# Kernel tuning notes

Measured on AMD Instinct MI355X. Metric: run time of the kernel, lower is better.

Reference implementation:

```python
import jax, jax.numpy as jnp
import numpy as np

EPS = 1e-5

def layer_norm(x, w, b):
    mu = x.mean(-1, keepdims=True)
    var = x.var(-1, keepdims=True)
    return (x - mu) / jnp.sqrt(var + EPS) * w + b

def moe_ffn(y, gW, W1, b1, W2, b2, topk):
    # y: [B,N,d]; W1: [E,d,f]; W2: [E,f,d].  Dense-equivalent of the
    # torch gather/compute/scatter-add dispatch: every expert runs on every
    # token, combined with top-k gate weights (zero for unselected experts).
    gate = jax.nn.softmax(y @ gW, axis=-1)                       # [B,N,E]
    w, sel = jax.lax.top_k(gate, topk)                           # [B,N,k]
    onehot = jax.nn.one_hot(sel, gW.shape[-1], dtype=y.dtype)    # [B,N,k,E]
    comb = jnp.einsum('bnk,bnke->bne', w, onehot)                # combine weights
    hmid = jax.nn.gelu(jnp.einsum('bnd,edf->bnef', y, W1) + b1, approximate=False)
    eo = jnp.einsum('bnef,efd->bned', hmid, W2) + b2             # [B,N,E,d]
    out = jnp.einsum('bne,bned->bnd', comb, eo)
    mask = onehot.sum(2)                                         # [B,N,E] 0/1
    cnt = mask.sum((0, 1))                                       # tokens per expert
    emb = jnp.einsum('bne,bnd->ed', mask, y) / jnp.maximum(cnt, 1.0)[:, None]
    return out, gate, emb

def setup_inputs():
    B, S, N = 8, 512, 1024
    d, H, E, f, L, topk = 512, 8, 8, 8, 2, 2   # d_ff == n_heads (repo quirk)
    key = jax.random.key(0)
    ks = iter(jax.random.split(key, 40))
    g = lambda shape, s=0.02: jax.random.normal(next(ks), shape, jnp.float32) * s
    return dict(
        x=jax.random.normal(next(ks), (B, S, N), jnp.float32),
        revin_w=jnp.ones((N,), jnp.float32) + g((N,), 0.01),
        revin_b=g((N,), 0.01),
        emb_W=g((S, d)), emb_b=g((d,)),
        Wq=g((L, d, d)), bq=g((L, d)),
        Wk=g((L, d, d)), bk=g((L, d)),
        Wv=g((L, d, d)), bv=g((L, d)),
        Wo=g((L, d, d)), bo=g((L, d)),
        ln1_w=jnp.ones((L, d), jnp.float32), ln1_b=jnp.zeros((L, d), jnp.float32),
        ln2_w=jnp.ones((L, d), jnp.float32), ln2_b=jnp.zeros((L, d), jnp.float32),
        gate_W=g((L, d, E)),
        eW1=g((L, E, d, f)), eb1=g((L, E, f)),
        eW2=g((L, E, f, d)), eb2=g((L, E, d)),
        enc_norm_w=jnp.ones((d,), jnp.float32), enc_norm_b=jnp.zeros((d,), jnp.float32),
        head_gate_W=g((d, E)),
        head_W=g((E, d, d)), head_b=g((E, d)),
        topk=topk, n_heads=H,
    )

def reference(x, revin_w, revin_b, emb_W, emb_b, Wq, bq, Wk, bk, Wv, bv, Wo, bo,
              ln1_w, ln1_b, ln2_w, ln2_b, gate_W, eW1, eb1, eW2, eb2,
              enc_norm_w, enc_norm_b, head_gate_W, head_W, head_b, topk, n_heads):
    B, S, N = x.shape
    d = emb_W.shape[1]
    H = n_heads
    dh = d // H
    L = Wq.shape[0]
    # RevIN normalize over time per variable (dropout layers are eval/identity)
    xv = jnp.swapaxes(x, 1, 2)                                   # [B,N,S]
    mean = xv.mean(-1, keepdims=True)
    std = jnp.sqrt(xv.var(-1, keepdims=True) + EPS)
    xn = (xv - mean) / std * revin_w[None, :, None] + revin_b[None, :, None]
    # DataEmbedding_inverted: Linear over the time axis -> variable tokens
    h = xn @ emb_W + emb_b                                       # [B,N,d]
    for l in range(L):
        q = (h @ Wq[l] + bq[l]).reshape(B, N, H, dh)
        k = (h @ Wk[l] + bk[l]).reshape(B, N, H, dh)
        v = (h @ Wv[l] + bv[l]).reshape(B, N, H, dh)
        attn = jax.nn.softmax(jnp.einsum('bnhe,bmhe->bhnm', q, k) / jnp.sqrt(jnp.float32(dh)), axis=-1)
        o = jnp.einsum('bhnm,bmhe->bnhe', attn, v).reshape(B, N, d) @ Wo[l] + bo[l]
        h = layer_norm(h + o, ln1_w[l], ln1_b[l])
        ffn, _gate, _emb = moe_ffn(h, gate_W[l], eW1[l], eb1[l], eW2[l], eb2[l], topk)
        h = layer_norm(h + ffn, ln2_w[l], ln2_b[l])
    h = layer_norm(h, enc_norm_w, enc_norm_b)
    # MoE projection head: experts are Linear(d, d)
    gate = jax.nn.softmax(h @ head_gate_W, axis=-1)
    w, sel = jax.lax.top_k(gate, topk)
    onehot = jax.nn.one_hot(sel, head_gate_W.shape[-1], dtype=h.dtype)
    comb = jnp.einsum('bnk,bnke->bne', w, onehot)
    eo = jnp.einsum('bnd,edf->bnef', h, head_W) + head_b         # [B,N,E,d]
    out = jnp.einsum('bne,bned->bnd', comb, eo)                  # [B,N,d]
    # RevIN denorm applied on [B, d_model, N]
    o2 = jnp.swapaxes(out, 1, 2)
    o2 = (o2 - revin_b[None, None, :]) / (revin_w[None, None, :] + 1e-10)
    o2 = o2 * jnp.swapaxes(std, 1, 2) + jnp.swapaxes(mean, 1, 2)
    return jnp.swapaxes(o2, 1, 2)                                # [B, n_vars, d_model]
```

## Files before the change

kernel.cpp:

```cpp
#include <hip/hip_runtime.h>
#include <math.h>

#define BATCH 8
#define SEQ 512
#define NVAR 1024
#define DM 512
#define NH 8
#define DH 64
#define NE 8
#define NF 8
#define NL 2
#define NTOK (BATCH*NVAR)
#define LN_EPS 1e-5f
#define LSC 2048.0f
#define ILSC (1.0f/2048.0f)

typedef __attribute__((ext_vector_type(8))) _Float16 f16x8;
typedef __attribute__((ext_vector_type(4))) float f32x4;
#define MFMA16 __builtin_amdgcn_mfma_f32_16x16x32_f16

__device__ __forceinline__ void fsplit(float v, _Float16& hi, _Float16& lo) {
    hi = (_Float16)v;
    lo = (_Float16)((v - (float)hi) * LSC);
}
__device__ __forceinline__ float frec(_Float16 hi, _Float16 lo) {
    return (float)hi + (float)lo * ILSC;
}

__device__ __forceinline__ void gload_lds16(const _Float16* g, _Float16* l) {
    __builtin_amdgcn_global_load_lds(
        (const __attribute__((address_space(1))) void*)g,
        (__attribute__((address_space(3))) void*)l, 16, 0, 0);
}

#define DPPROR(v, C) __int_as_float(__builtin_amdgcn_update_dpp(0, __float_as_int(v), (C), 0xF, 0xF, true))
__device__ __forceinline__ float rowmax16(float v) {
    v = fmaxf(v, DPPROR(v, 0x121));
    v = fmaxf(v, DPPROR(v, 0x122));
    v = fmaxf(v, DPPROR(v, 0x124));
    v = fmaxf(v, DPPROR(v, 0x128));
    return v;
}
__device__ __forceinline__ float rowsum16(float v) {
    v += DPPROR(v, 0x121);
    v += DPPROR(v, 0x122);
    v += DPPROR(v, 0x124);
    v += DPPROR(v, 0x128);
    return v;
}
// ... 123 lines not shown
            }
        }
    }
    #undef G_STAGE
#pragma unroll
    for (int h2 = 0; h2 < 2; ++h2)
#pragma unroll
        for (int nt = 0; nt < 4; ++nt) {
            int col = bn + nt*16 + m16;
            float bv = bias[col];
#pragma unroll
            for (int r = 0; r < 4; ++r) {
                size_t row = bm + w*32 + h2*16 + quad*4 + r;
                float v = a1[h2][nt][r] + a2[h2][nt][r]*ILSC + bv;
                if (C) C[row*N + col] = v;
                if (Chi) {
                    _Float16 h_, l_; fsplit(v, h_, l_);
                    Chi[row*N + col] = h_; Clo[row*N + col] = l_;
                }
            }
        }
}

__global__ __launch_bounds__(256) void gemm_qk_kernel(
        const _Float16* __restrict__ Ahg, const _Float16* __restrict__ Alg,
        const _Float16* __restrict__ Whg, const _Float16* __restrict__ Wlg,
        const float* __restrict__ biasQ, const float* __restrict__ biasK,
        _Float16* __restrict__ Qhi, _Float16* __restrict__ Qlo,
        _Float16* __restrict__ KKhi, _Float16* __restrict__ KKlo) {
    __shared__ _Float16 smem[24576];
    int id = blockIdx.x;
    int rm = ((id & 7) << 7) | (id >> 3);
    int bm = (rm >> 4) << 7, bn = (rm & 15) << 6;
    int t = threadIdx.x;
    int w = t >> 6, lane = t & 63, m16 = lane & 15, quad = lane >> 4;
    int wv = __builtin_amdgcn_readfirstlane(w);
    int lrow = lane >> 2, lcol = (lane & 3) << 3;
    f32x4 a1[2][4] = {}, a2[2][4] = {};

    #define G_STAGE(c, kk) do {                                              \
        _Pragma("unroll")                                                    \
        for (int ch = 0; ch < 2; ++ch) {                                     \
            size_t ga = (size_t)(bm + wv*32 + ch*16 + lrow)*DM + (kk) + lcol;\
            gload_lds16(&Ahg[ga], &smem[(c)*4096 + (wv*32 + ch*16)*32]);     \
            gload_lds16(&Alg[ga], &smem[8192 + (c)*4096 + (wv*32 + ch*16)*32]); \
        }                                                                    \
        size_t gb = (size_t)(bn + wv*16 + lrow)*DM + (kk) + lcol;            \
        gload_lds16(&Whg[gb], &smem[16384 + (c)*2048 + (wv*16)*32]);         \
        gload_lds16(&Wlg[gb], &smem[20480 + (c)*2048 + (wv*16)*32]);         \
    } while (0)

    G_STAGE(0, 0);
    int cur = 0;
    for (int k0 = 0; k0 < DM; k0 += 32, cur ^= 1) {
        __syncthreads();
        if (k0 + 32 < DM) G_STAGE(cur ^ 1, k0 + 32);
        const _Float16* AH = &smem[cur*4096];
        const _Float16* AL = &smem[8192 + cur*4096];
        const _Float16* BH = &smem[16384 + cur*2048];
        const _Float16* BL = &smem[20480 + cur*2048];
        f16x8 bh_[4], bl_[4];
#pragma unroll
        for (int nt = 0; nt < 4; ++nt) {
            bh_[nt] = *(const f16x8*)&BH[(nt*16 + m16)*32 + quad*8];
            bl_[nt] = *(const f16x8*)&BL[(nt*16 + m16)*32 + quad*8];
        }
#pragma unroll
        for (int h2 = 0; h2 < 2; ++h2) {
            f16x8 ah = *(const f16x8*)&AH[(w*32 + h2*16 + m16)*32 + quad*8];
            f16x8 al = *(const f16x8*)&AL[(w*32 + h2*16 + m16)*32 + quad*8];
#pragma unroll
            for (int nt = 0; nt < 4; ++nt) {
                a1[h2][nt] = MFMA16(ah, bh_[nt], a1[h2][nt], 0, 0, 0);
                a2[h2][nt] = MFMA16(ah, bl_[nt], a2[h2][nt], 0, 0, 0);
                a2[h2][nt] = MFMA16(al, bh_[nt], a2[h2][nt], 0, 0, 0);
            }
        }
    }
    #undef G_STAGE
    const float* bias = (bn < 512) ? biasQ : biasK;
    _Float16* Ohi = (bn < 512) ? Qhi : KKhi;
    _Float16* Olo = (bn < 512) ? Qlo : KKlo;
    int cb = (bn < 512) ? bn : bn - 512;
#pragma unroll
    for (int h2 = 0; h2 < 2; ++h2)
#pragma unroll
        for (int nt = 0; nt < 4; ++nt) {
            int col = cb + nt*16 + m16;
            float bv = bias[col];
#pragma unroll
            for (int r = 0; r < 4; ++r) {
                size_t row = bm + w*32 + h2*16 + quad*4 + r;
                float v = a1[h2][nt][r] + a2[h2][nt][r]*ILSC + bv;
                _Float16 h_, l_; fsplit(v, h_, l_);
                Ohi[row*DM + col] = h_; Olo[row*DM + col] = l_;
            }
        }
}

__global__ __launch_bounds__(256) void gemm_f16x2_vt_kernel(
        const _Float16* __restrict__ Ahg, const _Float16* __restrict__ Alg,
        const _Float16* __restrict__ Whg, const _Float16* __restrict__ Wlg,
        const float* __restrict__ bias,
        _Float16* __restrict__ vthi, _Float16* __restrict__ vtlo) {
    __shared__ _Float16 smem[24576];
    int id = blockIdx.x + (blockIdx.y << 3);
    int rm = ((id & 7) << 6) | (id >> 3);
    int bm = (rm >> 3) << 7, bn = (rm & 7) << 6;
    int t = threadIdx.x;
    int w = t >> 6, lane = t & 63, m16 = lane & 15, quad = lane >> 4;
    int wv = __builtin_amdgcn_readfirstlane(w);
    int lrow = lane >> 2, lcol = (lane & 3) << 3;
    f32x4 a1[2][4] = {}, a2[2][4] = {};

    #define G_STAGE(c, kk) do {                                              \
        _Pragma("unroll")                                                    \
        for (int ch = 0; ch < 2; ++ch) {                                     \
            size_t ga = (size_t)(bm + wv*32 + ch*16 + lrow)*DM + (kk) + lcol;\
            gload_lds16(&Ahg[ga], &smem[(c)*4096 + (wv*32 + ch*16)*32]);     \
            gload_lds16(&Alg[ga], &smem[8192 + (c)*4096 + (wv*32 + ch*16)*32]); \
        }                                                                    \
        size_t gb = (size_t)(bn + wv*16 + lrow)*DM + (kk) + lcol;            \
        gload_lds16(&Whg[gb], &smem[16384 + (c)*2048 + (wv*16)*32]);         \
        gload_lds16(&Wlg[gb], &smem[20480 + (c)*2048 + (wv*16)*32]);         \
    } while (0)

    G_STAGE(0, 0);
    int cur = 0;
    for (int k0 = 0; k0 < DM; k0 += 32, cur ^= 1) {
        __syncthreads();
        if (k0 + 32 < DM) G_STAGE(cur ^ 1, k0 + 32);
        const _Float16* AH = &smem[cur*4096];
        const _Float16* AL = &smem[8192 + cur*4096];
        const _Float16* BH = &smem[16384 + cur*2048];
        const _Float16* BL = &smem[20480 + cur*2048];
        f16x8 bh_[4], bl_[4];
#pragma unroll
        for (int nt = 0; nt < 4; ++nt) {
            bh_[nt] = *(const f16x8*)&BH[(nt*16 + m16)*32 + quad*8];
            bl_[nt] = *(const f16x8*)&BL[(nt*16 + m16)*32 + quad*8];
        }
#pragma unroll
        for (int h2 = 0; h2 < 2; ++h2) {
            f16x8 ah = *(const f16x8*)&AH[(w*32 + h2*16 + m16)*32 + quad*8];
            f16x8 al = *(const f16x8*)&AL[(w*32 + h2*16 + m16)*32 + quad*8];
#pragma unroll
            for (int nt = 0; nt < 4; ++nt) {
                a1[h2][nt] = MFMA16(ah, bh_[nt], a1[h2][nt], 0, 0, 0);
                a2[h2][nt] = MFMA16(ah, bl_[nt], a2[h2][nt], 0, 0, 0);
                a2[h2][nt] = MFMA16(al, bh_[nt], a2[h2][nt], 0, 0, 0);
            }
        }
    }
    #undef G_STAGE
    __syncthreads();
    float (*Ct)[65] = (float (*)[65])smem;
#pragma unroll
    for (int h2 = 0; h2 < 2; ++h2)
#pragma unroll
        for (int nt = 0; nt < 4; ++nt) {
            float bv = bias[bn + nt*16 + m16];
#pragma unroll
            for (int r = 0; r < 4; ++r)
                Ct[w*32 + h2*16 + quad*4 + r][nt*16 + m16] = a1[h2][nt][r] + a2[h2][nt][r]*ILSC + bv;
        }
    __syncthreads();
    int b = bm >> 10, tokn0 = bm & 1023, hh = bn >> 6;
    int dh = t >> 2, tg = (t & 3) << 4;
    size_t rowb = ((size_t)(b*8 + hh)*64 + dh)*NVAR + tokn0;
    for (int hb = 0; hb < 2; ++hb) {
        int tl0 = hb*64 + tg;
        unsigned short hbuf[16], lbuf[16];
#pragma unroll
        for (int i = 0; i < 16; ++i) {
            _Float16 h_, l_; fsplit(Ct[tl0 + i][dh], h_, l_);
            hbuf[i] = __builtin_bit_cast(unsigned short, h_);
            lbuf[i] = __builtin_bit_cast(unsigned short, l_);
        }
        uint4 uh0, uh1, ul0, ul1;
        uh0.x = hbuf[0]|(hbuf[1]<<16);  uh0.y = hbuf[2]|(hbuf[3]<<16);
        uh0.z = hbuf[4]|(hbuf[5]<<16);  uh0.w = hbuf[6]|(hbuf[7]<<16);
        uh1.x = hbuf[8]|(hbuf[9]<<16);  uh1.y = hbuf[10]|(hbuf[11]<<16);
        uh1.z = hbuf[12]|(hbuf[13]<<16);uh1.w = hbuf[14]|(hbuf[15]<<16);
        ul0.x = lbuf[0]|(lbuf[1]<<16);  ul0.y = lbuf[2]|(lbuf[3]<<16);
        ul0.z = lbuf[4]|(lbuf[5]<<16);  ul0.w = lbuf[6]|(lbuf[7]<<16);
        ul1.x = lbuf[8]|(lbuf[9]<<16);  ul1.y = lbuf[10]|(lbuf[11]<<16);
        ul1.z = lbuf[12]|(lbuf[13]<<16);ul1.w = lbuf[14]|(lbuf[15]<<16);
        *(uint4*)&vthi[rowb + tl0]     = uh0;
        *(uint4*)&vthi[rowb + tl0 + 8] = uh1;
        *(uint4*)&vtlo[rowb + tl0]     = ul0;
        *(uint4*)&vtlo[rowb + tl0 + 8] = ul1;
    }
}

__global__ __launch_bounds__(256, 4) void attn_f16x2_kernel(
        const _Float16* __restrict__ qh, const _Float16* __restrict__ ql,
        const _Float16* __restrict__ kh, const _Float16* __restrict__ kl,
        const _Float16* __restrict__ vth, const _Float16* __restrict__ vtl,
        _Float16* __restrict__ oh, _Float16* __restrict__ ol) {
    __shared__ _Float16 Kh[64][72], Kl[64][72];
    __shared__ _Float16 Vh[64][72], Vl[64][72];
    int blk = blockIdx.x;
    blk = ((blk & 7) << 7) | (blk >> 3);
    int qt = blk & 15, bh = blk >> 4;
    int b = bh >> 3, hh = bh & 7;
    int q0 = qt << 6;
    int t = threadIdx.x;
    int w = t >> 6, lane = t & 63;
    int m16 = lane & 15, quad = lane >> 4;
    size_t bbase = (size_t)b * NVAR;
    size_t vbase = (size_t)bh * DH * NVAR;

    f16x8 qfh[2], qfl[2];
#pragma unroll
// ... 49 lines not shown
        if (__any(grow)) {
#pragma unroll
            for (int r = 0; r < 4; ++r) {
                float mnew = fmaxf(mrow[r], mx[r]);
                float alpha = __expf(mrow[r] - mnew);
                mrow[r] = mnew;
                lrow[r] *= alpha;
#pragma unroll
                for (int nt = 0; nt < 4; ++nt) { o1[nt][r] *= alpha; o2[nt][r] *= alpha; }
            }
        }
#pragma unroll
        for (int r = 0; r < 4; ++r) {
            float p0 = __expf(pbuf[0][r] - mrow[r]);
            float p1 = __expf(pbuf[1][r] - mrow[r]);
            float p2 = __expf(pbuf[2][r] - mrow[r]);
            float p3 = __expf(pbuf[3][r] - mrow[r]);
            lrow[r] += rowsum16(p0 + p1 + p2 + p3);
            pbuf[0][r] = p0; pbuf[1][r] = p1; pbuf[2][r] = p2; pbuf[3][r] = p3;
        }
#pragma unroll
        for (int nt = 0; nt < 4; ++nt)
#pragma unroll
            for (int r = 0; r < 4; ++r) {
                _Float16 h_, l_; fsplit(pbuf[nt][r], h_, l_);
                Kh[w*16 + quad*4 + r][nt*16 + m16] = h_;
                Kl[w*16 + quad*4 + r][nt*16 + m16] = l_;
            }

#pragma unroll
        for (int ks = 0; ks < 2; ++ks) {
            f16x8 ph = *(const f16x8*)&Kh[w*16 + m16][ks*32 + quad*8];
            f16x8 pl = *(const f16x8*)&Kl[w*16 + m16][ks*32 + quad*8];
#pragma unroll
            for (int nt = 0; nt < 4; ++nt) {
                f16x8 vh_ = *(const f16x8*)&Vh[nt*16 + m16][ks*32 + quad*8];
                f16x8 vl_ = *(const f16x8*)&Vl[nt*16 + m16][ks*32 + quad*8];
                o1[nt] = MFMA16(ph, vh_, o1[nt], 0, 0, 0);
                o2[nt] = MFMA16(ph, vl_, o2[nt], 0, 0, 0);
                o2[nt] = MFMA16(pl, vh_, o2[nt], 0, 0, 0);
            }
        }
        __syncthreads();
    }
#pragma unroll
    for (int r = 0; r < 4; ++r) {
        float inv = 1.0f / lrow[r];
        size_t rowp = (bbase + q0 + w*16 + quad*4 + r)*DM + hh*DH;
#pragma unroll
        for (int nt = 0; nt < 4; ++nt) {
            float ov = fmaf(o2[nt][r], ILSC, o1[nt][r]) * inv;
            _Float16 h_, l_; fsplit(ov, h_, l_);
            oh[rowp + nt*16 + m16] = h_;
            ol[rowp + nt*16 + m16] = l_;
        }
    }
}

__global__ __launch_bounds__(256) void ln_kernel(
        _Float16* __restrict__ hhi, _Float16* __restrict__ hlo,
        const float* __restrict__ res,
        const float* __restrict__ w, const float* __restrict__ b) {
    int rowi = blockIdx.x, t = threadIdx.x;
    size_t base = (size_t)rowi * DM;
    int c = t << 1;
    unsigned int uh = *(const unsigned int*)&hhi[base + c];
    unsigned int ul = *(const unsigned int*)&hlo[base + c];
    _Float16 h0 = __builtin_bit_cast(_Float16, (unsigned short)(uh & 0xFFFF));
    _Float16 h1 = __builtin_bit_cast(_Float16, (unsigned short)(uh >> 16));
    _Float16 l0 = __builtin_bit_cast(_Float16, (unsigned short)(ul & 0xFFFF));
    _Float16 l1 = __builtin_bit_cast(_Float16, (unsigned short)(ul >> 16));
    float v0 = frec(h0, l0);
    float v1 = frec(h1, l1);
    if (res) { float2 rv = *(const float2*)&res[base + c]; v0 += rv.x; v1 += rv.y; }
    float s = v0 + v1, q = v0*v0 + v1*v1;
#pragma unroll
    for (int off = 1; off < 64; off <<= 1) {
        s += __shfl_xor(s, off);
        q += __shfl_xor(q, off);
    }
    __shared__ float sred[4], qred[4];
    int wid = t >> 6, lane = t & 63;
    if (lane == 0) { sred[wid] = s; qred[wid] = q; }
    __syncthreads();
    s = sred[0] + sred[1] + sred[2] + sred[3];
    q = qred[0] + qred[1] + qred[2] + qred[3];
    float m = s / (float)DM;
    float var = q / (float)DM - m*m;
    float inv = 1.0f / sqrtf(var + LN_EPS);
    float2 wv = *(const float2*)&w[c];
    float2 bv = *(const float2*)&b[c];
    float y0 = (v0 - m)*inv * wv.x + bv.x;
    float y1 = (v1 - m)*inv * wv.y + bv.y;
    _Float16 h0o, l0o, h1o, l1o;
    fsplit(y0, h0o, l0o); fsplit(y1, h1o, l1o);
    *(unsigned int*)&hhi[base + c] =
        (unsigned int)__builtin_bit_cast(unsigned short, h0o) |
        ((unsigned int)__builtin_bit_cast(unsigned short, h1o) << 16);
    *(unsigned int*)&hlo[base + c] =
        (unsigned int)__builtin_bit_cast(unsigned short, l0o) |
        ((unsigned int)__builtin_bit_cast(unsigned short, l1o) << 16);
}

__device__ __forceinline__ float gelu_exact(float xv) {
    return 0.5f * xv * (1.0f + erff(xv * 0.70710678118654752f));
}

__global__ __launch_bounds__(256) void moe_ln_kernel(
        _Float16* __restrict__ hhi, _Float16* __restrict__ hlo,
        const float* __restrict__ gW, const float* __restrict__ W1, const float* __restrict__ b1,
        const float* __restrict__ W2, const float* __restrict__ b2,
        const float* __restrict__ lw, const float* __restrict__ lb) {
    int tok = blockIdx.x, t = threadIdx.x;
    __shared__ float hs[DM];
    __shared__ float red[32][8];
    __shared__ float glog[8];
    __shared__ float hmid[8];
    __shared__ float wsel[2];
    __shared__ int   esel[2];
    __shared__ float sred[4], qred[4];
    size_t base = (size_t)tok * DM;
    int c = t << 1;
    unsigned int uh = *(const unsigned int*)&hhi[base + c];
    unsigned int ul = *(const unsigned int*)&hlo[base + c];
    float hv0 = frec(__builtin_bit_cast(_Float16, (unsigned short)(uh & 0xFFFF)),
                     __builtin_bit_cast(_Float16, (unsigned short)(ul & 0xFFFF)));
    float hv1 = frec(__builtin_bit_cast(_Float16, (unsigned short)(uh >> 16)),
                     __builtin_bit_cast(_Float16, (unsigned short)(ul >> 16)));
    hs[c] = hv0; hs[c + 1] = hv1;
    __syncthreads();
    int e = t & 7, i0 = t >> 3;
    {
        float a = 0.f;
        for (int i = i0; i < DM; i += 32) a += hs[i] * gW[i*NE + e];
        red[i0][e] = a;
    }
    __syncthreads();
    if (t < 8) { float sv = 0.f; for (int i = 0; i < 32; ++i) sv += red[i][t]; glog[t] = sv; }
    __syncthreads();
    if (t == 0) {
        float m0 = -1e30f, m1 = -1e30f; int s0i = 0, s1i = 0;
        for (int ei = 0; ei < 8; ++ei) {
            float vv = glog[ei];
            if (vv > m0) { m1 = m0; s1i = s0i; m0 = vv; s0i = ei; }
            else if (vv > m1) { m1 = vv; s1i = ei; }
        }
        float Z = 0.f;
        for (int ei = 0; ei < 8; ++ei) Z += expf(glog[ei] - m0);
        wsel[0] = 1.0f / Z;
        wsel[1] = expf(m1 - m0) / Z;
        esel[0] = s0i; esel[1] = s1i;
// ... 23 lines not shown
        }
        o0 += wk * s0v; o1 += wk * s1v;
        __syncthreads();
    }
    float v0 = hv0 + o0, v1 = hv1 + o1;
    float s = v0 + v1, q = v0*v0 + v1*v1;
#pragma unroll
    for (int off = 1; off < 64; off <<= 1) {
        s += __shfl_xor(s, off);
        q += __shfl_xor(q, off);
    }
    int wid = t >> 6, lane = t & 63;
    if (lane == 0) { sred[wid] = s; qred[wid] = q; }
    __syncthreads();
    s = sred[0] + sred[1] + sred[2] + sred[3];
    q = qred[0] + qred[1] + qred[2] + qred[3];
    float m = s / (float)DM;
    float var = q / (float)DM - m*m;
    float inv = 1.0f / sqrtf(var + LN_EPS);
    float2 wv = *(const float2*)&lw[c];
    float2 bv = *(const float2*)&lb[c];
    float y0 = (v0 - m)*inv * wv.x + bv.x;
    float y1 = (v1 - m)*inv * wv.y + bv.y;
    _Float16 h0o, l0o, h1o, l1o;
    fsplit(y0, h0o, l0o); fsplit(y1, h1o, l1o);
    *(unsigned int*)&hhi[base + c] =
        (unsigned int)__builtin_bit_cast(unsigned short, h0o) |
        ((unsigned int)__builtin_bit_cast(unsigned short, h1o) << 16);
    *(unsigned int*)&hlo[base + c] =
        (unsigned int)__builtin_bit_cast(unsigned short, l0o) |
        ((unsigned int)__builtin_bit_cast(unsigned short, l1o) << 16);
}

__global__ __launch_bounds__(256) void encln_gate_kernel(
        _Float16* __restrict__ hhi, _Float16* __restrict__ hlo,
        const float* __restrict__ lw, const float* __restrict__ lb,
        const float* __restrict__ gW,
        int* __restrict__ sel, float2* __restrict__ wpair) {
    int tok = blockIdx.x, t = threadIdx.x;
    __shared__ float hs[DM];
    __shared__ float red[32][8];
    __shared__ float glog[8];
    __shared__ float sred[4], qred[4];
    size_t base = (size_t)tok * DM;
    int c = t << 1;
    unsigned int uh = *(const unsigned int*)&hhi[base + c];
    unsigned int ul = *(const unsigned int*)&hlo[base + c];
    float v0 = frec(__builtin_bit_cast(_Float16, (unsigned short)(uh & 0xFFFF)),
                    __builtin_bit_cast(_Float16, (unsigned short)(ul & 0xFFFF)));
    float v1 = frec(__builtin_bit_cast(_Float16, (unsigned short)(uh >> 16)),
                    __builtin_bit_cast(_Float16, (unsigned short)(ul >> 16)));
    float s = v0 + v1, q = v0*v0 + v1*v1;
#pragma unroll
    for (int off = 1; off < 64; off <<= 1) {
        s += __shfl_xor(s, off);
        q += __shfl_xor(q, off);
    }
    int wid = t >> 6, lane = t & 63;
    if (lane == 0) { sred[wid] = s; qred[wid] = q; }
    __syncthreads();
    s = sred[0] + sred[1] + sred[2] + sred[3];
    q = qred[0] + qred[1] + qred[2] + qred[3];
    float m = s / (float)DM;
    float var = q / (float)DM - m*m;
    float inv = 1.0f / sqrtf(var + LN_EPS);
    float2 wv = *(const float2*)&lw[c];
    float2 bv = *(const float2*)&lb[c];
    float y0 = (v0 - m)*inv * wv.x + bv.x;
    float y1 = (v1 - m)*inv * wv.y + bv.y;
    _Float16 h0o, l0o, h1o, l1o;
    fsplit(y0, h0o, l0o); fsplit(y1, h1o, l1o);
    *(unsigned int*)&hhi[base + c] =
        (unsigned int)__builtin_bit_cast(unsigned short, h0o) |
        ((unsigned int)__builtin_bit_cast(unsigned short, h1o) << 16);
    *(unsigned int*)&hlo[base + c] =
        (unsigned int)__builtin_bit_cast(unsigned short, l0o) |
        ((unsigned int)__builtin_bit_cast(unsigned short, l1o) << 16);
    hs[c] = y0; hs[c + 1] = y1;
    __syncthreads();
    int e = t & 7, i0 = t >> 3;
    float a = 0.f;
    for (int i = i0; i < DM; i += 32) a += hs[i] * gW[i*NE + e];
    red[i0][e] = a;
    __syncthreads();
    if (t < 8) { float sv = 0.f; for (int i = 0; i < 32; ++i) sv += red[i][t]; glog[t] = sv; }
    __syncthreads();
    if (t == 0) {
        float m0 = -1e30f, m1 = -1e30f; int s0i = 0, s1i = 0;
        for (int ei = 0; ei < 8; ++ei) {
            float vv = glog[ei];
            if (vv > m0) { m1 = m0; s1i = s0i; m0 = vv; s0i = ei; }
            else if (vv > m1) { m1 = vv; s1i = ei; }
        }
        float Z = 0.f;
        for (int ei = 0; ei < 8; ++ei) Z += __expf(glog[ei] - m0);
        float2 wvv;
        wvv.x = 1.0f / Z;
        wvv.y = __expf(m1 - m0) / Z;
        sel[tok] = s0i | (s1i << 3);
        wpair[tok] = wvv;
    }
}

__global__ __launch_bounds__(64) void head_init_kernel(int* __restrict__ cnt) {
    if (threadIdx.x < NE) cnt[threadIdx.x] = 0;
}

__global__ __launch_bounds__(64) void head_bucket_kernel(
        const int* __restrict__ sel, const float2* __restrict__ wpair,
        int* __restrict__ cnt, int* __restrict__ idxlist, float* __restrict__ wlist,
        int* __restrict__ pos0, int* __restrict__ pos1) {
    int lane = threadIdx.x;
    int tok = blockIdx.x*64 + lane;
    int s = sel[tok];
    int s0 = s & 7, s1 = (s >> 3) & 7;
    float2 wv = wpair[tok];
    unsigned long long lmask = (lane == 63) ? 0x7FFFFFFFFFFFFFFFull
                                            : ((1ull << lane) - 1ull);
#pragma unroll
    for (int e = 0; e < NE; ++e) {
        unsigned long long m0 = __ballot(s0 == e);
        unsigned long long m1 = __ballot(s1 == e);
        int tot = __popcll(m0) + __popcll(m1);
        int basep = 0;
        if (lane == 0 && tot > 0) basep = atomicAdd(&cnt[e], tot);
        basep = __shfl(basep, 0);
        if (s0 == e) {
            int p = basep + __popcll(m0 & lmask);
// ... 184 lines not shown
    dim3 ggemm(DM/64, NTOK/128);

    revin_stats_kernel<<<dim3(BATCH*16), blk, 0, stream>>>(x, mean, stdd);
    revin_norm_kernel<<<dim3(NVAR/32, SEQ/32, BATCH), blk, 0, stream>>>(
        x, mean, stdd, revin_w, revin_b, qhi, qlo);

    WSrcs srcs;
    srcs.p[0] = emb_W;
    for (int l = 0; l < NL; ++l) {
        srcs.p[1 + l*4 + 0] = Wq + (size_t)l*DM*DM;
        srcs.p[1 + l*4 + 1] = Wk + (size_t)l*DM*DM;
        srcs.p[1 + l*4 + 2] = Wv + (size_t)l*DM*DM;
        srcs.p[1 + l*4 + 3] = Wo + (size_t)l*DM*DM;
    }
    transpose_w_kernel<<<dim3(8, 8, 9), blk, 0, stream>>>(srcs, whi, wlo);

    gemm_f16x2_kernel<<<ggemm, blk, 0, stream>>>(
        qhi, qlo, whi, wlo, emb_b, nullptr, hhi, hlo, NTOK, SEQ, DM);

    for (int l = 0; l < NL; ++l) {
        size_t oq = (size_t)(1 + l*4 + 0)*DM*DM;
        size_t ov = (size_t)(1 + l*4 + 2)*DM*DM;
        size_t oo = (size_t)(1 + l*4 + 3)*DM*DM;
        gemm_qk_kernel<<<dim3(1024), blk, 0, stream>>>(
            hhi, hlo, whi + oq, wlo + oq, bq + l*DM, bk + l*DM,
            qhi, qlo, khi, klo);
        gemm_f16x2_vt_kernel<<<ggemm, blk, 0, stream>>>(
            hhi, hlo, whi + ov, wlo + ov, bv + l*DM, vthi, vtlo);
        attn_f16x2_kernel<<<dim3(64*16), blk, 0, stream>>>(
            qhi, qlo, khi, klo, vthi, vtlo, qhi, qlo);
        gemm_f16x2_kernel<<<ggemm, blk, 0, stream>>>(
            qhi, qlo, whi + oo, wlo + oo, bo + l*DM, proj, nullptr, nullptr, NTOK, DM, DM);
        ln_kernel<<<dim3(NTOK), blk, 0, stream>>>(hhi, hlo, proj, ln1_w + l*DM, ln1_b + l*DM);
        moe_ln_kernel<<<dim3(NTOK), blk, 0, stream>>>(
            hhi, hlo, gate_W + (size_t)l*DM*NE,
            eW1 + (size_t)l*NE*DM*NF, eb1 + (size_t)l*NE*NF,
            eW2 + (size_t)l*NE*NF*DM, eb2 + (size_t)l*NE*DM,
            ln2_w + l*DM, ln2_b + l*DM);
    }

    WSrcs hsrcs;
    for (int e = 0; e < NE; ++e) hsrcs.p[e] = hW + (size_t)e*DM*DM;
    hsrcs.p[8] = hW;
    transpose_w_kernel<<<dim3(8, 8, 8), blk, 0, stream>>>(hsrcs, vthi, vtlo);

    head_init_kernel<<<dim3(1), dim3(64), 0, stream>>>(cnt);
    encln_gate_kernel<<<dim3(NTOK), blk, 0, stream>>>(
        hhi, hlo, enc_w, enc_b, hgW, sel, wpair);
    head_bucket_kernel<<<dim3(NTOK/64), dim3(64), 0, stream>>>(
        sel, wpair, cnt, idxlist, wlist, pos0, pos1);
    head_prefix_kernel<<<dim3(1), dim3(64), 0, stream>>>(cnt);
    head_gemm_f16x2_kernel<<<dim3(576), blk, 0, stream>>>(
        hhi, hlo, vthi, vtlo, hb, cnt, idxlist, wlist, slotf);
    head_combine_kernel<<<dim3(NTOK), blk, 0, stream>>>(
        slotf, pos0, pos1, cnt, revin_w, revin_b, mean, stdd, out);
}
```

Before: 812.3 us.

## Fuse QK and V projection GEMMs into one launch, pack f16 splits

Merges the Q/K GEMM and the transposed-V GEMM into a single kernel that chooses its path by block index, removing one launch per layer and improving tail occupancy. Replaces scalar hi/lo f16 splitting with packed cvt_pkrtz conversions in the attention, layernorm and gate kernels. Folds the expert-counter zeroing into the encoder-norm gate kernel, dropping a tiny launch. The packed conversion rounds toward zero, which slightly changes the hi/lo split.

```diff
diff --git a/kernel.cpp b/kernel.cpp
--- a/kernel.cpp
+++ b/kernel.cpp
@@ -16,6 +16,7 @@
 #define ILSC (1.0f/2048.0f)
 
 typedef __attribute__((ext_vector_type(8))) _Float16 f16x8;
+typedef __attribute__((ext_vector_type(2))) _Float16 f16x2;
 typedef __attribute__((ext_vector_type(4))) float f32x4;
 #define MFMA16 __builtin_amdgcn_mfma_f32_16x16x32_f16
 
@@ -25,6 +26,11 @@
 }
 __device__ __forceinline__ float frec(_Float16 hi, _Float16 lo) {
     return (float)hi + (float)lo * ILSC;
+}
+__device__ __forceinline__ void fsplit2(float a, float b, f16x2& h2, f16x2& l2) {
+    h2 = __builtin_bit_cast(f16x2, __builtin_amdgcn_cvt_pkrtz(a, b));
+    l2 = __builtin_bit_cast(f16x2, __builtin_amdgcn_cvt_pkrtz(
+             (a - (float)h2.x)*LSC, (b - (float)h2.y)*LSC));
 }
 
 __device__ __forceinline__ void gload_lds16(const _Float16* g, _Float16* l) {
@@ -194,174 +200,167 @@
         }
 }
 
-__global__ __launch_bounds__(256) void gemm_qk_kernel(
+__global__ __launch_bounds__(256) void gemm_qkvt_kernel(
         const _Float16* __restrict__ Ahg, const _Float16* __restrict__ Alg,
-        const _Float16* __restrict__ Whg, const _Float16* __restrict__ Wlg,
+        const _Float16* __restrict__ Wqkh, const _Float16* __restrict__ Wqkl,
+        const _Float16* __restrict__ Wvh,  const _Float16* __restrict__ Wvl,
         const float* __restrict__ biasQ, const float* __restrict__ biasK,
+        const float* __restrict__ biasV,
         _Float16* __restrict__ Qhi, _Float16* __restrict__ Qlo,
-        _Float16* __restrict__ KKhi, _Float16* __restrict__ KKlo) {
+        _Float16* __restrict__ KKhi, _Float16* __restrict__ KKlo,
+        _Float16* __restrict__ vthi, _Float16* __restrict__ vtlo) {
     __shared__ _Float16 smem[24576];
-    int id = blockIdx.x;
-    int rm = ((id & 7) << 7) | (id >> 3);
-    int bm = (rm >> 4) << 7, bn = (rm & 15) << 6;
     int t = threadIdx.x;
     int w = t >> 6, lane = t & 63, m16 = lane & 15, quad = lane >> 4;
     int wv = __builtin_amdgcn_readfirstlane(w);
     int lrow = lane >> 2, lcol = (lane & 3) << 3;
-    f32x4 a1[2][4] = {}, a2[2][4] = {};
-
-    #define G_STAGE(c, kk) do {                                              \
-        _Pragma("unroll")                                                    \
-        for (int ch = 0; ch < 2; ++ch) {                                     \
-            size_t ga = (size_t)(bm + wv*32 + ch*16 + lrow)*DM + (kk) + lcol;\
-            gload_lds16(&Ahg[ga], &smem[(c)*4096 + (wv*32 + ch*16)*32]);     \
-            gload_lds16(&Alg[ga], &smem[8192 + (c)*4096 + (wv*32 + ch*16)*32]); \
-        }                                                                    \
-        size_t gb = (size_t)(bn + wv*16 + lrow)*DM + (kk) + lcol;            \
-        gload_lds16(&Whg[gb], &smem[16384 + (c)*2048 + (wv*16)*32]);         \
-        gload_lds16(&Wlg[gb], &smem[20480 + (c)*2048 + (wv*16)*32]);         \
-    } while (0)
-
-    G_STAGE(0, 0);
-    int cur = 0;
-    for (int k0 = 0; k0 < DM; k0 += 32, cur ^= 1) {
-        __syncthreads();
-        if (k0 + 32 < DM) G_STAGE(cur ^ 1, k0 + 32);
-        const _Float16* AH = &smem[cur*4096];
-        const _Float16* AL = &smem[8192 + cur*4096];
-        const _Float16* BH = &smem[16384 + cur*2048];
-        const _Float16* BL = &smem[20480 + cur*2048];
-        f16x8 bh_[4], bl_[4];
-#pragma unroll
-        for (int nt = 0; nt < 4; ++nt) {
-            bh_[nt] = *(const f16x8*)&BH[(nt*16 + m16)*32 + quad*8];
-            bl_[nt] = *(const f16x8*)&BL[(nt*16 + m16)*32 + quad*8];
-        }
-#pragma unroll
-        for (int h2 = 0; h2 < 2; ++h2) {
-            f16x8 ah = *(const f16x8*)&AH[(w*32 + h2*16 + m16)*32 + quad*8];
-            f16x8 al = *(const f16x8*)&AL[(w*32 + h2*16 + m16)*32 + quad*8];
+
+    if (blockIdx.x < 1024) {
+        int id = blockIdx.x;
+        int rm = ((id & 7) << 7) | (id >> 3);
+        int bm = (rm >> 4) << 7, bn = (rm & 15) << 6;
+        f32x4 a1[2][4] = {}, a2[2][4] = {};
+        #define QK_STAGE(c, kk) do {                                             \
+            _Pragma("unroll")                                                    \
+            for (int ch = 0; ch < 2; ++ch) {                                     \
+                size_t ga = (size_t)(bm + wv*32 + ch*16 + lrow)*DM + (kk) + lcol;\
+                gload_lds16(&Ahg[ga], &smem[(c)*4096 + (wv*32 + ch*16)*32]);     \
+                gload_lds16(&Alg[ga], &smem[8192 + (c)*4096 + (wv*32 + ch*16)*32]); \
+            }                                                                    \
+            size_t gb = (size_t)(bn + wv*16 + lrow)*DM + (kk) + lcol;            \
+            gload_lds16(&Wqkh[gb], &smem[16384 + (c)*2048 + (wv*16)*32]);        \
+            gload_lds16(&Wqkl[gb], &smem[20480 + (c)*2048 + (wv*16)*32]);        \
+        } while (0)
+        QK_STAGE(0, 0);
+        int cur = 0;
+        for (int k0 = 0; k0 < DM; k0 += 32, cur ^= 1) {
+            __syncthreads();
+            if (k0 + 32 < DM) QK_STAGE(cur ^ 1, k0 + 32);
+            const _Float16* AH = &smem[cur*4096];
+            const _Float16* AL = &smem[8192 + cur*4096];
+            const _Float16* BH = &smem[16384 + cur*2048];
+            const _Float16* BL = &smem[20480 + cur*2048];
+            f16x8 bh_[4], bl_[4];
 #pragma unroll
             for (int nt = 0; nt < 4; ++nt) {
-                a1[h2][nt] = MFMA16(ah, bh_[nt], a1[h2][nt], 0, 0, 0);
-                a2[h2][nt] = MFMA16(ah, bl_[nt], a2[h2][nt], 0, 0, 0);
-                a2[h2][nt] = MFMA16(al, bh_[nt], a2[h2][nt], 0, 0, 0);
-            }
-        }
-    }
-    #undef G_STAGE
-    const float* bias = (bn < 512) ? biasQ : biasK;
-    _Float16* Ohi = (bn < 512) ? Qhi : KKhi;
-    _Float16* Olo = (bn < 512) ? Qlo : KKlo;
-    int cb = (bn < 512) ? bn : bn - 512;
-#pragma unroll
-    for (int h2 = 0; h2 < 2; ++h2)
-#pragma unroll
-        for (int nt = 0; nt < 4; ++nt) {
-            int col = cb + nt*16 + m16;
-            float bv = bias[col];
-#pragma unroll
-            for (int r = 0; r < 4; ++r) {
-                size_t row = bm + w*32 + h2*16 + quad*4 + r;
-                float v = a1[h2][nt][r] + a2[h2][nt][r]*ILSC + bv;
-                _Float16 h_, l_; fsplit(v, h_, l_);
-                Ohi[row*DM + col] = h_; Olo[row*DM + col] = l_;
-            }
-        }
-}
-
-__global__ __launch_bounds__(256) void gemm_f16x2_vt_kernel(
-        const _Float16* __restrict__ Ahg, const _Float16* __restrict__ Alg,
-        const _Float16* __restrict__ Whg, const _Float16* __restrict__ Wlg,
-        const float* __restrict__ bias,
-        _Float16* __restrict__ vthi, _Float16* __restrict__ vtlo) {
-    __shared__ _Float16 smem[24576];
-    int id = blockIdx.x + (blockIdx.y << 3);
-    int rm = ((id & 7) << 6) | (id >> 3);
-    int bm = (rm >> 3) << 7, bn = (rm & 7) << 6;
-    int t = threadIdx.x;
-    int w = t >> 6, lane = t & 63, m16 = lane & 15, quad = lane >> 4;
-    int wv = __builtin_amdgcn_readfirstlane(w);
-    int lrow = lane >> 2, lcol = (lane & 3) << 3;
-    f32x4 a1[2][4] = {}, a2[2][4] = {};
-
-    #define G_STAGE(c, kk) do {                                              \
-        _Pragma("unroll")                                                    \
-        for (int ch = 0; ch < 2; ++ch) {                                     \
-            size_t ga = (size_t)(bm + wv*32 + ch*16 + lrow)*DM + (kk) + lcol;\
-            gload_lds16(&Ahg[ga], &smem[(c)*4096 + (wv*32 + ch*16)*32]);     \
-            gload_lds16(&Alg[ga], &smem[8192 + (c)*4096 + (wv*32 + ch*16)*32]); \
-        }                                                                    \
-        size_t gb = (size_t)(bn + wv*16 + lrow)*DM + (kk) + lcol;            \
-        gload_lds16(&Whg[gb], &smem[16384 + (c)*2048 + (wv*16)*32]);         \
-        gload_lds16(&Wlg[gb], &smem[20480 + (c)*2048 + (wv*16)*32]);         \
-    } while (0)
-
-    G_STAGE(0, 0);
-    int cur = 0;
-    for (int k0 = 0; k0 < DM; k0 += 32, cur ^= 1) {
-        __syncthreads();
-        if (k0 + 32 < DM) G_STAGE(cur ^ 1, k0 + 32);
-        const _Float16* AH = &smem[cur*4096];
-        const _Float16* AL = &smem[8192 + cur*4096];
-        const _Float16* BH = &smem[16384 + cur*2048];
-        const _Float16* BL = &smem[20480 + cur*2048];
-        f16x8 bh_[4], bl_[4];
-#pragma unroll
-        for (int nt = 0; nt < 4; ++nt) {
-            bh_[nt] = *(const f16x8*)&BH[(nt*16 + m16)*32 + quad*8];
-            bl_[nt] = *(const f16x8*)&BL[(nt*16 + m16)*32 + quad*8];
-        }
-#pragma unroll
-        for (int h2 = 0; h2 < 2; ++h2) {
-            f16x8 ah = *(const f16x8*)&AH[(w*32 + h2*16 + m16)*32 + quad*8];
-            f16x8 al = *(const f16x8*)&AL[(w*32 + h2*16 + m16)*32 + quad*8];
+                bh_[nt] = *(const f16x8*)&BH[(nt*16 + m16)*32 + quad*8];
+                bl_[nt] = *(const f16x8*)&BL[(nt*16 + m16)*32 + quad*8];
+            }
+#pragma unroll
+            for (int h2 = 0; h2 < 2; ++h2) {
+                f16x8 ah = *(const f16x8*)&AH[(w*32 + h2*16 + m16)*32 + quad*8];
+                f16x8 al = *(const f16x8*)&AL[(w*32 + h2*16 + m16)*32 + quad*8];
+#pragma unroll
+                for (int nt = 0; nt < 4; ++nt) {
+                    a1[h2][nt] = MFMA16(ah, bh_[nt], a1[h2][nt], 0, 0, 0);
+                    a2[h2][nt] = MFMA16(ah, bl_[nt], a2[h2][nt], 0, 0, 0);
+                    a2[h2][nt] = MFMA16(al, bh_[nt], a2[h2][nt], 0, 0, 0);
+                }
+            }
+        }
+        #undef QK_STAGE
+        const float* bias = (bn < 512) ? biasQ : biasK;
+        _Float16* Ohi = (bn < 512) ? Qhi : KKhi;
+        _Float16* Olo = (bn < 512) ? Qlo : KKlo;
+        int cb = (bn < 512) ? bn : bn - 512;
+#pragma unroll
+        for (int h2 = 0; h2 < 2; ++h2)
 #pragma unroll
             for (int nt = 0; nt < 4; ++nt) {
-                a1[h2][nt] = MFMA16(ah, bh_[nt], a1[h2][nt], 0, 0, 0);
-                a2[h2][nt] = MFMA16(ah, bl_[nt], a2[h2][nt], 0, 0, 0);
-                a2[h2][nt] = MFMA16(al, bh_[nt], a2[h2][nt], 0, 0, 0);
-            }
-        }
-    }
-    #undef G_STAGE
-    __syncthreads();
-    float (*Ct)[65] = (float (*)[65])smem;
-#pragma unroll
-    for (int h2 = 0; h2 < 2; ++h2)
-#pragma unroll
-        for (int nt = 0; nt < 4; ++nt) {
-            float bv = bias[bn + nt*16 + m16];
-#pragma unroll
-            for (int r = 0; r < 4; ++r)
-                Ct[w*32 + h2*16 + quad*4 + r][nt*16 + m16] = a1[h2][nt][r] + a2[h2][nt][r]*ILSC + bv;
-        }
-    __syncthreads();
-    int b = bm >> 10, tokn0 = bm & 1023, hh = bn >> 6;
-    int dh = t >> 2, tg = (t & 3) << 4;
-    size_t rowb = ((size_t)(b*8 + hh)*64 + dh)*NVAR + tokn0;
-    for (int hb = 0; hb < 2; ++hb) {
-        int tl0 = hb*64 + tg;
-        unsigned short hbuf[16], lbuf[16];
-#pragma unroll
-        for (int i = 0; i < 16; ++i) {
-            _Float16 h_, l_; fsplit(Ct[tl0 + i][dh], h_, l_);
-            hbuf[i] = __builtin_bit_cast(unsigned short, h_);
-            lbuf[i] = __builtin_bit_cast(unsigned short, l_);
-        }
-        uint4 uh0, uh1, ul0, ul1;
-        uh0.x = hbuf[0]|(hbuf[1]<<16);  uh0.y = hbuf[2]|(hbuf[3]<<16);
-        uh0.z = hbuf[4]|(hbuf[5]<<16);  uh0.w = hbuf[6]|(hbuf[7]<<16);
-        uh1.x = hbuf[8]|(hbuf[9]<<16);  uh1.y = hbuf[10]|(hbuf[11]<<16);
-        uh1.z = hbuf[12]|(hbuf[13]<<16);uh1.w = hbuf[14]|(hbuf[15]<<16);
-        ul0.x = lbuf[0]|(lbuf[1]<<16);  ul0.y = lbuf[2]|(lbuf[3]<<16);
-        ul0.z = lbuf[4]|(lbuf[5]<<16);  ul0.w = lbuf[6]|(lbuf[7]<<16);
-        ul1.x = lbuf[8]|(lbuf[9]<<16);  ul1.y = lbuf[10]|(lbuf[11]<<16);
-        ul1.z = lbuf[12]|(lbuf[13]<<16);ul1.w = lbuf[14]|(lbuf[15]<<16);
-        *(uint4*)&vthi[rowb + tl0]     = uh0;
-        *(uint4*)&vthi[rowb + tl0 + 8] = uh1;
-        *(uint4*)&vtlo[rowb + tl0]     = ul0;
-        *(uint4*)&vtlo[rowb + tl0 + 8] = ul1;
+                int col = cb + nt*16 + m16;
+                float bv = bias[col];
+#pragma unroll
+                for (int r = 0; r < 4; ++r) {
+                    size_t row = bm + w*32 + h2*16 + quad*4 + r;
+                    float v = a1[h2][nt][r] + a2[h2][nt][r]*ILSC + bv;
+                    _Float16 h_, l_; fsplit(v, h_, l_);
+                    Ohi[row*DM + col] = h_; Olo[row*DM + col] = l_;
+                }
+            }
+        return;
+    }
+    {
+        int id = blockIdx.x - 1024;
+        int rm = ((id & 7) << 6) | (id >> 3);
+        int bm = (rm >> 3) << 7, bn = (rm & 7) << 6;
+        f32x4 a1[2][4] = {}, a2[2][4] = {};
+        #define VT_STAGE(c, kk) do {                                             \
+            _Pragma("unroll")                                                    \
+            for (int ch = 0; ch < 2; ++ch) {                                     \
+                size_t ga = (size_t)(bm + wv*32 + ch*16 + lrow)*DM + (kk) + lcol;\
+                gload_lds16(&Ahg[ga], &smem[(c)*4096 + (wv*32 + ch*16)*32]);     \
+                gload_lds16(&Alg[ga], &smem[8192 + (c)*4096 + (wv*32 + ch*16)*32]); \
+            }                                                                    \
+            size_t gb = (size_t)(bn + wv*16 + lrow)*DM + (kk) + lcol;            \
+            gload_lds16(&Wvh[gb], &smem[16384 + (c)*2048 + (wv*16)*32]);         \
+            gload_lds16(&Wvl[gb], &smem[20480 + (c)*2048 + (wv*16)*32]);         \
+        } while (0)
+        VT_STAGE(0, 0);
+        int cur = 0;
+        for (int k0 = 0; k0 < DM; k0 += 32, cur ^= 1) {
+            __syncthreads();
+            if (k0 + 32 < DM) VT_STAGE(cur ^ 1, k0 + 32);
+            const _Float16* AH = &smem[cur*4096];
+            const _Float16* AL = &smem[8192 + cur*4096];
+            const _Float16* BH = &smem[16384 + cur*2048];
+            const _Float16* BL = &smem[20480 + cur*2048];
+            f16x8 bh_[4], bl_[4];
+#pragma unroll
+            for (int nt = 0; nt < 4; ++nt) {
+                bh_[nt] = *(const f16x8*)&BH[(nt*16 + m16)*32 + quad*8];
+                bl_[nt] = *(const f16x8*)&BL[(nt*16 + m16)*32 + quad*8];
+            }
+#pragma unroll
+            for (int h2 = 0; h2 < 2; ++h2) {
+                f16x8 ah = *(const f16x8*)&AH[(w*32 + h2*16 + m16)*32 + quad*8];
+                f16x8 al = *(const f16x8*)&AL[(w*32 + h2*16 + m16)*32 + quad*8];
+#pragma unroll
+                for (int nt = 0; nt < 4; ++nt) {
+                    a1[h2][nt] = MFMA16(ah, bh_[nt], a1[h2][nt], 0, 0, 0);
+                    a2[h2][nt] = MFMA16(ah, bl_[nt], a2[h2][nt], 0, 0, 0);
+                    a2[h2][nt] = MFMA16(al, bh_[nt], a2[h2][nt], 0, 0, 0);
+                }
+            }
+        }
+        #undef VT_STAGE
+        __syncthreads();
+        float (*Ct)[65] = (float (*)[65])smem;
+#pragma unroll
+        for (int h2 = 0; h2 < 2; ++h2)
+#pragma unroll
+            for (int nt = 0; nt < 4; ++nt) {
+                float bv = biasV[bn + nt*16 + m16];
+#pragma unroll
+                for (int r = 0; r < 4; ++r)
+                    Ct[w*32 + h2*16 + quad*4 + r][nt*16 + m16] = a1[h2][nt][r] + a2[h2][nt][r]*ILSC + bv;
+            }
+        __syncthreads();
+        int b = bm >> 10, tokn0 = bm & 1023, hh = bn >> 6;
+        int dh = t >> 2, tg = (t & 3) << 4;
+        size_t rowb = ((size_t)(b*8 + hh)*64 + dh)*NVAR + tokn0;
+        for (int hb = 0; hb < 2; ++hb) {
+            int tl0 = hb*64 + tg;
+            unsigned short hbuf[16], lbuf[16];
+#pragma unroll
+            for (int i = 0; i < 16; ++i) {
+                _Float16 h_, l_; fsplit(Ct[tl0 + i][dh], h_, l_);
+                hbuf[i] = __builtin_bit_cast(unsigned short, h_);
+                lbuf[i] = __builtin_bit_cast(unsigned short, l_);
+            }
+            uint4 uh0, uh1, ul0, ul1;
+            uh0.x = hbuf[0]|(hbuf[1]<<16);  uh0.y = hbuf[2]|(hbuf[3]<<16);
+            uh0.z = hbuf[4]|(hbuf[5]<<16);  uh0.w = hbuf[6]|(hbuf[7]<<16);
+            uh1.x = hbuf[8]|(hbuf[9]<<16);  uh1.y = hbuf[10]|(hbuf[11]<<16);
+            uh1.z = hbuf[12]|(hbuf[13]<<16);uh1.w = hbuf[14]|(hbuf[15]<<16);
+            ul0.x = lbuf[0]|(lbuf[1]<<16);  ul0.y = lbuf[2]|(lbuf[3]<<16);
+            ul0.z = lbuf[4]|(lbuf[5]<<16);  ul0.w = lbuf[6]|(lbuf[7]<<16);
+            ul1.x = lbuf[8]|(lbuf[9]<<16);  ul1.y = lbuf[10]|(lbuf[11]<<16);
+            ul1.z = lbuf[12]|(lbuf[13]<<16);ul1.w = lbuf[14]|(lbuf[15]<<16);
+            *(uint4*)&vthi[rowb + tl0]     = uh0;
+            *(uint4*)&vthi[rowb + tl0 + 8] = uh1;
+            *(uint4*)&vtlo[rowb + tl0]     = ul0;
+            *(uint4*)&vtlo[rowb + tl0 + 8] = ul1;
+        }
     }
 }
 
@@ -457,10 +456,13 @@
 #pragma unroll
         for (int nt = 0; nt < 4; ++nt)
 #pragma unroll
-            for (int r = 0; r < 4; ++r) {
-                _Float16 h_, l_; fsplit(pbuf[nt][r], h_, l_);
-                Kh[w*16 + quad*4 + r][nt*16 + m16] = h_;
-                Kl[w*16 + quad*4 + r][nt*16 + m16] = l_;
+            for (int rp = 0; rp < 2; ++rp) {
+                f16x2 h2, l2;
+                fsplit2(pbuf[nt][2*rp], pbuf[nt][2*rp + 1], h2, l2);
+                Kh[w*16 + quad*4 + 2*rp][nt*16 + m16]     = h2.x;
+                Kh[w*16 + quad*4 + 2*rp + 1][nt*16 + m16] = h2.y;
+                Kl[w*16 + quad*4 + 2*rp][nt*16 + m16]     = l2.x;
+                Kl[w*16 + quad*4 + 2*rp + 1][nt*16 + m16] = l2.y;
             }
 
 #pragma unroll
@@ -482,12 +484,18 @@
     for (int r = 0; r < 4; ++r) {
         float inv = 1.0f / lrow[r];
         size_t rowp = (bbase + q0 + w*16 + quad*4 + r)*DM + hh*DH;
-#pragma unroll
-        for (int nt = 0; nt < 4; ++nt) {
-            float ov = fmaf(o2[nt][r], ILSC, o1[nt][r]) * inv;
-            _Float16 h_, l_; fsplit(ov, h_, l_);
-            oh[rowp + nt*16 + m16] = h_;
-            ol[rowp + nt*16 + m16] = l_;
+        float ovv[4];
+#pragma unroll
+        for (int nt = 0; nt < 4; ++nt)
+            ovv[nt] = fmaf(o2[nt][r], ILSC, o1[nt][r]) * inv;
+#pragma unroll
+        for (int np = 0; np < 2; ++np) {
+            f16x2 h2, l2;
+            fsplit2(ovv[2*np], ovv[2*np + 1], h2, l2);
+            oh[rowp + (2*np)*16 + m16]     = h2.x;
+            oh[rowp + (2*np + 1)*16 + m16] = h2.y;
+            ol[rowp + (2*np)*16 + m16]     = l2.x;
+            ol[rowp + (2*np + 1)*16 + m16] = l2.y;
         }
     }
 }
@@ -499,14 +507,10 @@
     int rowi = blockIdx.x, t = threadIdx.x;
     size_t base = (size_t)rowi * DM;
     int c = t << 1;
-    unsigned int uh = *(const unsigned int*)&hhi[base + c];
-    unsigned int ul = *(const unsigned int*)&hlo[base + c];
-    _Float16 h0 = __builtin_bit_cast(_Float16, (unsigned short)(uh & 0xFFFF));
-    _Float16 h1 = __builtin_bit_cast(_Float16, (unsigned short)(uh >> 16));
-    _Float16 l0 = __builtin_bit_cast(_Float16, (unsigned short)(ul & 0xFFFF));
-    _Float16 l1 = __builtin_bit_cast(_Float16, (unsigned short)(ul >> 16));
-    float v0 = frec(h0, l0);
-    float v1 = frec(h1, l1);
+    f16x2 hv = *(const f16x2*)&hhi[base + c];
+    f16x2 lv = *(const f16x2*)&hlo[base + c];
+    float v0 = frec(hv.x, lv.x);
+    float v1 = frec(hv.y, lv.y);
     if (res) { float2 rv = *(const float2*)&res[base + c]; v0 += rv.x; v1 += rv.y; }
     float s = v0 + v1, q = v0*v0 + v1*v1;
 #pragma unroll
@@ -527,14 +531,9 @@
     float2 bv = *(const float2*)&b[c];
     float y0 = (v0 - m)*inv * wv.x + bv.x;
     float y1 = (v1 - m)*inv * wv.y + bv.y;
-    _Float16 h0o, l0o, h1o, l1o;
-    fsplit(y0, h0o, l0o); fsplit(y1, h1o, l1o);
-    *(unsigned int*)&hhi[base + c] =
-        (unsigned int)__builtin_bit_cast(unsigned short, h0o) |
-        ((unsigned int)__builtin_bit_cast(unsigned short, h1o) << 16);
-    *(unsigned int*)&hlo[base + c] =
-        (unsigned int)__builtin_bit_cast(unsigned short, l0o) |
-        ((unsigned int)__builtin_bit_cast(unsigned short, l1o) << 16);
+    f16x2 h2, l2; fsplit2(y0, y1, h2, l2);
+    *(f16x2*)&hhi[base + c] = h2;
+    *(f16x2*)&hlo[base + c] = l2;
 }
 
 __device__ __forceinline__ float gelu_exact(float xv) {
@@ -556,12 +555,10 @@
     __shared__ float sred[4], qred[4];
     size_t base = (size_t)tok * DM;
     int c = t << 1;
-    unsigned int uh = *(const unsigned int*)&hhi[base + c];
-    unsigned int ul = *(const unsigned int*)&hlo[base + c];
-    float hv0 = frec(__builtin_bit_cast(_Float16, (unsigned short)(uh & 0xFFFF)),
-                     __builtin_bit_cast(_Float16, (unsigned short)(ul & 0xFFFF)));
-    float hv1 = frec(__builtin_bit_cast(_Float16, (unsigned short)(uh >> 16)),
-                     __builtin_bit_cast(_Float16, (unsigned short)(ul >> 16)));
+    f16x2 hv = *(const f16x2*)&hhi[base + c];
+    f16x2 lv = *(const f16x2*)&hlo[base + c];
+    float hv0 = frec(hv.x, lv.x);
+    float hv1 = frec(hv.y, lv.y);
     hs[c] = hv0; hs[c + 1] = hv1;
     __syncthreads();
     int e = t & 7, i0 = t >> 3;
@@ -631,34 +628,29 @@
     float2 bv = *(const float2*)&lb[c];
     float y0 = (v0 - m)*inv * wv.x + bv.x;
     float y1 = (v1 - m)*inv * wv.y + bv.y;
-    _Float16 h0o, l0o, h1o, l1o;
-    fsplit(y0, h0o, l0o); fsplit(y1, h1o, l1o);
-    *(unsigned int*)&hhi[base + c] =
-        (unsigned int)__builtin_bit_cast(unsigned short, h0o) |
-        ((unsigned int)__builtin_bit_cast(unsigned short, h1o) << 16);
-    *(unsigned int*)&hlo[base + c] =
-        (unsigned int)__builtin_bit_cast(unsigned short, l0o) |
-        ((unsigned int)__builtin_bit_cast(unsigned short, l1o) << 16);
+    f16x2 h2o, l2o; fsplit2(y0, y1, h2o, l2o);
+    *(f16x2*)&hhi[base + c] = h2o;
+    *(f16x2*)&hlo[base + c] = l2o;
 }
 
 __global__ __launch_bounds__(256) void encln_gate_kernel(
         _Float16* __restrict__ hhi, _Float16* __restrict__ hlo,
         const float* __restrict__ lw, const float* __restrict__ lb,
         const float* __restrict__ gW,
-        int* __restrict__ sel, float2* __restrict__ wpair) {
+        int* __restrict__ sel, float2* __restrict__ wpair,
+        int* __restrict__ cnt) {
     int tok = blockIdx.x, t = threadIdx.x;
+    if (tok == 0 && t < NE) cnt[t] = 0;
     __shared__ float hs[DM];
     __shared__ float red[32][8];
     __shared__ float glog[8];
     __shared__ float sred[4], qred[4];
     size_t base = (size_t)tok * DM;
     int c = t << 1;
-    unsigned int uh = *(const unsigned int*)&hhi[base + c];
-    unsigned int ul = *(const unsigned int*)&hlo[base + c];
-    float v0 = frec(__builtin_bit_cast(_Float16, (unsigned short)(uh & 0xFFFF)),
-                    __builtin_bit_cast(_Float16, (unsigned short)(ul & 0xFFFF)));
-    float v1 = frec(__builtin_bit_cast(_Float16, (unsigned short)(uh >> 16)),
-                    __builtin_bit_cast(_Float16, (unsigned short)(ul >> 16)));
+    f16x2 hv = *(const f16x2*)&hhi[base + c];
+    f16x2 lv = *(const f16x2*)&hlo[base + c];
+    float v0 = frec(hv.x, lv.x);
+    float v1 = frec(hv.y, lv.y);
     float s = v0 + v1, q = v0*v0 + v1*v1;
 #pragma unroll
     for (int off = 1; off < 64; off <<= 1) {
@@ -677,14 +669,9 @@
     float2 bv = *(const float2*)&lb[c];
     float y0 = (v0 - m)*inv * wv.x + bv.x;
     float y1 = (v1 - m)*inv * wv.y + bv.y;
-    _Float16 h0o, l0o, h1o, l1o;
-    fsplit(y0, h0o, l0o); fsplit(y1, h1o, l1o);
-    *(unsigned int*)&hhi[base + c] =
-        (unsigned int)__builtin_bit_cast(unsigned short, h0o) |
-        ((unsigned int)__builtin_bit_cast(unsigned short, h1o) << 16);
-    *(unsigned int*)&hlo[base + c] =
-        (unsigned int)__builtin_bit_cast(unsigned short, l0o) |
-        ((unsigned int)__builtin_bit_cast(unsigned short, l1o) << 16);
+    f16x2 h2o, l2o; fsplit2(y0, y1, h2o, l2o);
+    *(f16x2*)&hhi[base + c] = h2o;
+    *(f16x2*)&hlo[base + c] = l2o;
     hs[c] = y0; hs[c + 1] = y1;
     __syncthreads();
     int e = t & 7, i0 = t >> 3;
@@ -709,10 +696,6 @@
         sel[tok] = s0i | (s1i << 3);
         wpair[tok] = wvv;
     }
-}
-
-__global__ __launch_bounds__(64) void head_init_kernel(int* __restrict__ cnt) {
-    if (threadIdx.x < NE) cnt[threadIdx.x] = 0;
 }
 
 __global__ __launch_bounds__(64) void head_bucket_kernel(
@@ -943,11 +926,10 @@
         size_t oq = (size_t)(1 + l*4 + 0)*DM*DM;
         size_t ov = (size_t)(1 + l*4 + 2)*DM*DM;
         size_t oo = (size_t)(1 + l*4 + 3)*DM*DM;
-        gemm_qk_kernel<<<dim3(1024), blk, 0, stream>>>(
-            hhi, hlo, whi + oq, wlo + oq, bq + l*DM, bk + l*DM,
-            qhi, qlo, khi, klo);
-        gemm_f16x2_vt_kernel<<<ggemm, blk, 0, stream>>>(
-            hhi, hlo, whi + ov, wlo + ov, bv + l*DM, vthi, vtlo);
+        gemm_qkvt_kernel<<<dim3(1536), blk, 0, stream>>>(
+            hhi, hlo, whi + oq, wlo + oq, whi + ov, wlo + ov,
+            bq + l*DM, bk + l*DM, bv + l*DM,
+            qhi, qlo, khi, klo, vthi, vtlo);
         attn_f16x2_kernel<<<dim3(64*16), blk, 0, stream>>>(
             qhi, qlo, khi, klo, vthi, vtlo, qhi, qlo);
         gemm_f16x2_kernel<<<ggemm, blk, 0, stream>>>(
@@ -965,9 +947,8 @@
     hsrcs.p[8] = hW;
     transpose_w_kernel<<<dim3(8, 8, 8), blk, 0, stream>>>(hsrcs, vthi, vtlo);
 
-    head_init_kernel<<<dim3(1), dim3(64), 0, stream>>>(cnt);
     encln_gate_kernel<<<dim3(NTOK), blk, 0, stream>>>(
-        hhi, hlo, enc_w, enc_b, hgW, sel, wpair);
+        hhi, hlo, enc_w, enc_b, hgW, sel, wpair, cnt);
     head_bucket_kernel<<<dim3(NTOK/64), dim3(64), 0, stream>>>(
         sel, wpair, cnt, idxlist, wlist, pos0, pos1);
     head_prefix_kernel<<<dim3(1), dim3(64), 0, stream>>>(cnt);
```

New measurement: 813.5 us. Within noise of the previous version (+0.2%).
